# Optimization experiments

Hardware: AMD Instinct MI355X
Metric: run time of the kernel (lower is better)

## Reference

```python
import jax, jax.numpy as jnp
import numpy as np
from jax.scipy.special import logsumexp

D, V, B, N = 256, 10000, 16, 22
CF, CR, CA = 400, 120, 48   # num_func_cats, num_res_cats, num_arg_cats
NEG = -1e9


def setup_inputs() -> dict:
    key = jax.random.key(0)
    ks = jax.random.split(key, 12)
    s = 0.1
    return {
        "fake_emb": jnp.eye(CR, dtype=jnp.float32),  # nn.Parameter(torch.eye(num_res_cats))
        "nt_emb": jax.random.normal(ks[0], (CF, D), jnp.float32),
        "rule_W": jax.random.normal(ks[1], (2 * CA, CR), jnp.float32) * s,
        "rule_b": jnp.zeros((2 * CA,), jnp.float32),
        "root_w": jax.random.normal(ks[2], (CF,), jnp.float32) * s,  # root_mlp weight (input dim 1)
        "root_b": jnp.zeros((CF,), jnp.float32),
        "root_mask": jnp.zeros((CF,), jnp.float32),  # can_be_root mask (0 = allowed)
        "split_W1": jax.random.normal(ks[3], (D, D), jnp.float32) * s,
        "split_b1": jnp.zeros((D,), jnp.float32),
        "res_W": jax.random.normal(ks[4], (2, 2, D, D), jnp.float32) * s,  # 2 ResidualLayers x 2 Linears
        "res_b": jnp.zeros((2, 2, D), jnp.float32),
        "split_Wo": jax.random.normal(ks[5], (D, 2), jnp.float32) * s,
        "split_bo": jnp.zeros((2,), jnp.float32),
        "emit_W": jax.random.normal(ks[6], (D, V), jnp.float32) * s,  # word emission head
        "emit_b": jnp.zeros((V,), jnp.float32),
        "words": jax.random.randint(ks[7], (B, N), 0, V),
        "lfunc_ixs": jax.random.randint(ks[8], (CR, CA), 0, CF),
        "rfunc_ixs": jax.random.randint(ks[9], (CR, CA), 0, CF),
    }


def reference(fake_emb, nt_emb, rule_W, rule_b, root_w, root_b, root_mask,
              split_W1, split_b1, res_W, res_b, split_Wo, split_bo,
              emit_W, emit_b, words, lfunc_ixs, rfunc_ixs):
    # ---- grammar scores (set_grammar branch) ----
    # root_mlp(eye(1)).squeeze() == root_w + root_b
    root_scores = jax.nn.log_softmax(root_mask + root_w + root_b)          # [CF]
    rule_scores = jax.nn.log_softmax(fake_emb @ rule_W.T + rule_b, axis=1)  # [CR, 2*CA]

    # split_mlp: Linear -> ResidualLayer x2 -> Linear(D,2)
    h = nt_emb @ split_W1 + split_b1
    for i in range(2):  # fixed small layer loop
        t = jax.nn.relu(h @ res_W[i, 0] + res_b[i, 0])
        h = jax.nn.relu(t @ res_W[i, 1] + res_b[i, 1]) + h
    split_scores = jax.nn.log_softmax(h @ split_Wo + split_bo, axis=1)      # [CF, 2]

    gL = rule_scores[:, :CA] + split_scores[:CR, 0:1]  # full_G_larg [CR, CA]
    gR = rule_scores[:, CA:] + split_scores[:CR, 0:1]  # full_G_rarg [CR, CA]

    # ---- emission model: log p(word | category) gathered per token ----
    word_lp = jax.nn.log_softmax(nt_emb @ emit_W + emit_b, axis=-1)  # [CF, V]
    emit = word_lp[:, words]                                         # [CF, B, N]
    term = (split_scores[:, 1][:, None, None] + emit).transpose(2, 1, 0)  # [N, B, CF]

    # ---- CKY inside pass: beta[i, j, b, cat] over spans ----
    beta = jnp.full((N, N, B, CF), NEG, jnp.float32)
    d = jnp.arange(N)
    beta = beta.at[d, d].set(term)

    for w in range(2, N + 1):  # recurrence over span widths (static)
        S = N - w + 1
        st = np.arange(S)[:, None]          # span starts [S,1]
        kk = np.arange(1, w)[None, :]       # split points [1,w-1]
        left = beta[st, st + kk - 1]                                   # [S,w-1,B,CF]
        right = beta[st + kk, np.broadcast_to(st + w - 1, (S, w - 1))]  # [S,w-1,B,CF]
        # res -> arg(left) + rfunc(right)
        sL = gL + left[..., :CA][..., None, :] + right[..., rfunc_ixs]  # [S,w-1,B,CR,CA]
        # res -> lfunc(left) + arg(right)
        sR = gR + left[..., lfunc_ixs] + right[..., :CA][..., None, :]
        new = jnp.logaddexp(logsumexp(sL, axis=(1, 4)),
                            logsumexp(sR, axis=(1, 4)))                 # [S,B,CR]
        full = jnp.full((S, B, CF), NEG, jnp.float32).at[..., :CR].set(new)
        beta = beta.at[st[:, 0], st[:, 0] + w - 1].set(full)

    ll = logsumexp(root_scores + beta[0, N - 1], axis=-1)  # [B]
    return -ll  # logprob_list * -1
```

## Files before the change

kernel.cpp:

```cpp
#include <hip/hip_runtime.h>
#include <math.h>

#define D 256
#define V 10000
#define BB 16
#define NN 22
#define CF 400
#define CR 120
#define CA 48
#define CRP 121
#define PADF 20

#define RT 8
#define MLPB 200
__global__ __launch_bounds__(512) void k_mlp_emit(const float* __restrict__ nt_emb,
                      const float* __restrict__ W1, const float* __restrict__ b1,
                      const float* __restrict__ resW, const float* __restrict__ resb,
                      const float* __restrict__ Wo, const float* __restrict__ bo,
                      const float* __restrict__ emit_W, const float* __restrict__ emit_b,
                      float* __restrict__ split_scores, float* __restrict__ partial) {
  int bid = blockIdx.x;
  int t = threadIdx.x;
  if (bid < MLPB) {
    __shared__ float xs[2][D], hs[2][D], ts[2][D], prt[2][2][D];
    __shared__ float redg[2][4][2];
    int c = t & 255; int h = t >> 8;
    int f0 = bid * 2;
    xs[h][c] = nt_emb[(size_t)(f0 + h) * D + c];
    __syncthreads();
    int d0 = h * 128;
    float a0 = 0.f, a1 = 0.f;
#pragma unroll 8
    for (int dd = 0; dd < 128; dd++) {
      float wv = W1[(size_t)(d0 + dd) * D + c];
      a0 += xs[0][d0 + dd] * wv; a1 += xs[1][d0 + dd] * wv;
    }
    prt[0][h][c] = a0; prt[1][h][c] = a1;
    __syncthreads();
    if (h == 0) {
      float bv = b1[c];
      hs[0][c] = prt[0][0][c] + prt[0][1][c] + bv;
      hs[1][c] = prt[1][0][c] + prt[1][1][c] + bv;
    }
    __syncthreads();
    for (int il = 0; il < 2; il++) {
      const float* W = resW + (size_t)(il * 2) * D * D;
      a0 = 0.f; a1 = 0.f;
#pragma unroll 8
      for (int dd = 0; dd < 128; dd++) {
        float wv = W[(size_t)(d0 + dd) * D + c];
        a0 += hs[0][d0 + dd] * wv; a1 += hs[1][d0 + dd] * wv;
      }
      prt[0][h][c] = a0; prt[1][h][c] = a1;
      __syncthreads();
      if (h == 0) {
        float bv = resb[(il * 2) * D + c];
        ts[0][c] = fmaxf(prt[0][0][c] + prt[0][1][c] + bv, 0.f);
        ts[1][c] = fmaxf(prt[1][0][c] + prt[1][1][c] + bv, 0.f);
      }
      __syncthreads();
      const float* W2 = resW + (size_t)(il * 2 + 1) * D * D;
      a0 = 0.f; a1 = 0.f;
#pragma unroll 8
      for (int dd = 0; dd < 128; dd++) {
        float wv = W2[(size_t)(d0 + dd) * D + c];
        a0 += ts[0][d0 + dd] * wv; a1 += ts[1][d0 + dd] * wv;
      }
      prt[0][h][c] = a0; prt[1][h][c] = a1;
      __syncthreads();
      if (h == 0) {
        float bv = resb[(il * 2 + 1) * D + c];
        hs[0][c] = fmaxf(prt[0][0][c] + prt[0][1][c] + bv, 0.f) + hs[0][c];
        hs[1][c] = fmaxf(prt[1][0][c] + prt[1][1][c] + bv, 0.f) + hs[1][c];
      }
      __syncthreads();
    }
    float y0 = hs[h][c] * Wo[c * 2 + 0], y1 = hs[h][c] * Wo[c * 2 + 1];
    for (int off = 32; off; off >>= 1) { y0 += __shfl_down(y0, off, 64); y1 += __shfl_down(y1, off, 64); }
    int wq = (t >> 6) & 3;
    if ((t & 63) == 0) { redg[h][wq][0] = y0; redg[h][wq][1] = y1; }
    __syncthreads();
    if (c == 0) {
      float s0 = redg[h][0][0] + redg[h][1][0] + redg[h][2][0] + redg[h][3][0] + bo[0];
      float s1 = redg[h][0][1] + redg[h][1][1] + redg[h][2][1] + redg[h][3][1] + bo[1];
      float m = fmaxf(s0, s1);
      float z = m + __logf(__expf(s0 - m) + __expf(s1 - m));
      split_scores[(f0 + h) * 2 + 0] = s0 - z;
      split_scores[(f0 + h) * 2 + 1] = s1 - z;
    }
  } else {
    __shared__ float exs[RT][D];
    __shared__ float ldsw[RT][8];
    int e = bid - MLPB;
    int y = e / 50;
    int xt = e % 50;
    int f0 = xt * RT;
    int v0 = y * 2048 + t * 4;
    for (int idx = t; idx < RT * D; idx += 512) {
      int ri = idx >> 8, d = idx & 255;
      exs[ri][d] = nt_emb[(size_t)(f0 + ri) * D + d];
    }
    __syncthreads();
    float psum[RT];
    for (int ri = 0; ri < RT; ri++) psum[ri] = 0.f;
    if (v0 < V) {
      float acc[RT][4];
#pragma unroll
      for (int ri = 0; ri < RT; ri++)
        for (int j = 0; j < 4; j++) acc[ri][j] = 0.f;
      for (int d4 = 0; d4 < D / 4; d4++) {
        float4 w0 = *(const float4*)(emit_W + (size_t)(4 * d4 + 0) * V + v0);
        float4 w1 = *(const float4*)(emit_W + (size_t)(4 * d4 + 1) * V + v0);
        float4 w2 = *(const float4*)(emit_W + (size_t)(4 * d4 + 2) * V + v0);
        float4 w3 = *(const float4*)(emit_W + (size_t)(4 * d4 + 3) * V + v0);
#pragma unroll
        for (int ri = 0; ri < RT; ri++) {
          float4 xv = *(const float4*)(&exs[ri][4 * d4]);
          acc[ri][0] += xv.x * w0.x + xv.y * w1.x + xv.z * w2.x + xv.w * w3.x;
          acc[ri][1] += xv.x * w0.y + xv.y * w1.y + xv.z * w2.y + xv.w * w3.y;
          acc[ri][2] += xv.x * w0.z + xv.y * w1.z + xv.z * w2.z + xv.w * w3.z;
          acc[ri][3] += xv.x * w0.w + xv.y * w1.w + xv.z * w2.w + xv.w * w3.w;
        }
      }
      float4 eb = *(const float4*)(emit_b + v0);
#pragma unroll
      for (int ri = 0; ri < RT; ri++)
        psum[ri] = __expf(acc[ri][0] + eb.x) + __expf(acc[ri][1] + eb.y) +
                   __expf(acc[ri][2] + eb.z) + __expf(acc[ri][3] + eb.w);
    }
    int lane = t & 63, wid = t >> 6;
    for (int ri = 0; ri < RT; ri++) {
      float v = psum[ri];
      for (int off = 32; off; off >>= 1) v += __shfl_down(v, off, 64);
      if (lane == 0) ldsw[ri][wid] = v;
    }
    __syncthreads();
    if (t < RT) {
      float s = 0.f;
      for (int wv = 0; wv < 8; wv++) s += ldsw[t][wv];
      partial[(f0 + t) * 8 + y] = s;
    }
  }
}

__global__ void k_glgr(const float* __restrict__ rule_W, const float* __restrict__ rule_b,
                       const float* __restrict__ split_scores,
                       const int* __restrict__ lf, const int* __restrict__ rf,
                       const float* __restrict__ partialE, float* __restrict__ logZ,
                       float4* __restrict__ rules) {
  __shared__ float red[128];
  __shared__ float shv[96];
  int r = blockIdx.x;
  int t = threadIdx.x;
  if (r == CR) {
    for (int f = t; f < CF; f += 128) {
      float s = 0.f;
      for (int ct = 0; ct < 5; ct++) s += partialE[f * 8 + ct];
      logZ[f] = __logf(s);
    }
    return;
  }
  float x = (t < 96) ? (rule_W[t * CR + r] + rule_b[t]) : -INFINITY;
  red[t] = x; __syncthreads();
  for (int off = 64; off; off >>= 1) { if (t < off) red[t] = fmaxf(red[t], red[t + off]); __syncthreads(); }
  float m = red[0]; __syncthreads();
  red[t] = (t < 96) ? __expf(x - m) : 0.f; __syncthreads();
  for (int off = 64; off; off >>= 1) { if (t < off) red[t] += red[t + off]; __syncthreads(); }
  float z = m + __logf(red[0]);
  float s0 = split_scores[r * 2 + 0];
  if (t < 96) shv[t] = __expf((x - z) + s0);
  __syncthreads();
  if (t < CA) {
    float4 pk;
    pk.x = shv[t];
    pk.y = shv[CA + t];
    pk.z = __int_as_float(rf[r * CA + t]);
    pk.w = __int_as_float(lf[r * CA + t]);
    rules[r * CA + t] = pk;
  }
}

__global__ __launch_bounds__(512) void k_term(const float* __restrict__ nt_emb,
                       const float* __restrict__ emit_W,
                       const float* __restrict__ emit_b, const int* __restrict__ words,
                       const float* __restrict__ split_scores, const float* __restrict__ logZ,
                       float* __restrict__ ET, float* __restrict__ bmax) {
  __shared__ float vals[CF];
  __shared__ float redw[8];
  __shared__ float mfin;
  int blk = blockIdx.x;
  int b = blk / NN, n = blk % NN;
  int t = threadIdx.x;
  int lane = t & 63, wid = t >> 6;
  int wd = words[b * NN + n];
  float wc0 = emit_W[(size_t)(4 * lane + 0) * V + wd];
  float wc1 = emit_W[(size_t)(4 * lane + 1) * V + wd];
  float wc2 = emit_W[(size_t)(4 * lane + 2) * V + wd];
  float wc3 = emit_W[(size_t)(4 * lane + 3) * V + wd];
  float eb = emit_b[wd];
  float vmax = -INFINITY;
  int fbase = wid * 50;
  for (int k = 0; k < 50; k += 2) {
    int f0 = fbase + k, f1 = f0 + 1;
    float4 xa = *(const float4*)(nt_emb + (size_t)f0 * D + 4 * lane);
    float4 xb = *(const float4*)(nt_emb + (size_t)f1 * D + 4 * lane);
    float va = xa.x * wc0 + xa.y * wc1 + xa.z * wc2 + xa.w * wc3;
    float vb = xb.x * wc0 + xb.y * wc1 + xb.z * wc2 + xb.w * wc3;
    for (int off = 32; off; off >>= 1) {
      va += __shfl_down(va, off, 64);
      vb += __shfl_down(vb, off, 64);
    }
    if (lane == 0) {
      float fa = split_scores[f0 * 2 + 1] + (va + eb) - logZ[f0];
      float fb = split_scores[f1 * 2 + 1] + (vb + eb) - logZ[f1];
      vals[f0] = fa; vals[f1] = fb;
      vmax = fmaxf(vmax, fmaxf(fa, fb));
    }
  }
  if (lane == 0) redw[wid] = vmax;
  __syncthreads();
  if (t == 0) {
    float m = redw[0];
    for (int i2 = 1; i2 < 8; i2++) m = fmaxf(m, redw[i2]);
    mfin = m;
    bmax[(n * NN + n) * BB + b] = m;
  }
  __syncthreads();
  float m = mfin;
  for (int f = t; f < CF; f += 512) ET[((size_t)n * CF + f) * BB + b] = __expf(vals[f] - m);
}

__global__ __launch_bounds__(512) void k_cky_part(const float4* __restrict__ rules,
                      const float* __restrict__ ET, const float* __restrict__ EB,
                      const float* __restrict__ bmax, float* __restrict__ partial,
                      int w, int rsplit) {
  __shared__ float SL[CF * PADF];
  __shared__ float SR[CF * PADF];
  __shared__ float sMbuf[21 * BB];
  __shared__ float cks[BB];
  __shared__ float4 sred[512];
  int t = threadIdx.x;
  int blk = blockIdx.x;
  int rb = blk % rsplit; int rem = blk / rsplit;
  int wm1 = w - 1;
  int k = rem % wm1; int s = rem / wm1;
  int i = s, j = s + w - 1;
  bool ld = (k == 0), rd = (k == wm1 - 1);
  if (t < BB * wm1) {
    int k2 = t >> 4, b2 = t & 15;
    sMbuf[t] = bmax[(i * NN + (i + k2)) * BB + b2] + bmax[((i + k2 + 1) * NN + j) * BB + b2];
  }
  __syncthreads();
  if (t < BB) {
    float M = sMbuf[t];
    for (int k2 = 1; k2 < wm1; k2++) M = fmaxf(M, sMbuf[k2 * BB + t]);
    cks[t] = __expf(sMbuf[k * BB + t] - M);
  }
  const float* srcL = ld ? (ET + (size_t)i * CF * BB) : (EB + (size_t)(i * NN + (i + k)) * CRP * BB);
  const float* srcR = rd ? (ET + (size_t)j * CF * BB) : (EB + (size_t)((i + k + 1) * NN + j) * CRP * BB);
  int rowsL = ld ? CF : CRP, rowsR = rd ? CF : CRP;
  for (int idx = t; idx < rowsL * 4; idx += 512) {
    int f = idx >> 2, q = idx & 3;
    *(float4*)&SL[f * PADF + q * 4] = *(const float4*)&srcL[f * BB + q * 4];
  }
  for (int idx = t; idx < rowsR * 4; idx += 512) {
    int f = idx >> 2, q = idx & 3;
    *(float4*)&SR[f * PADF + q * 4] = *(const float4*)&srcR[f * BB + q * 4];
  }
  __syncthreads();
  int nr = CR / rsplit;
  int asplit = 128 / nr;
  int bq = t & 3, rr = t >> 2;
  float4 acc = {0.f, 0.f, 0.f, 0.f};
  bool act = (rr < nr * asplit);
  int rloc = rr % nr, asub = rr / nr;
  int r = rb * nr + rloc;
  if (act) {
    int na = CA / asplit;
    const float4* rp = rules + (size_t)r * CA + asub * na;
    int boff = bq * 4;
    int aB = asub * na;
#pragma unroll 4
    for (int a0 = 0; a0 < na; a0++) {
      float4 rule = rp[a0];
      int a = aB + a0;
      int fL = __float_as_int(rule.z);
      int fR = __float_as_int(rule.w);
      int fLc = rd ? fL : min(fL, 120);
      int fRc = ld ? fR : min(fR, 120);
      float4 La = *(const float4*)&SL[a * PADF + boff];
      float4 Ra = *(const float4*)&SR[a * PADF + boff];
      float4 Rg = *(const float4*)&SR[fLc * PADF + boff];
      float4 Lg = *(const float4*)&SL[fRc * PADF + boff];
      acc.x += rule.x * (La.x * Rg.x) + rule.y * (Lg.x * Ra.x);
      acc.y += rule.x * (La.y * Rg.y) + rule.y * (Lg.y * Ra.y);
      acc.z += rule.x * (La.z * Rg.z) + rule.y * (Lg.z * Ra.z);
      acc.w += rule.x * (La.w * Rg.w) + rule.y * (Lg.w * Ra.w);
    }
  }
  if (asplit > 1) {
    sred[t] = acc;
    __syncthreads();
    if (act && asub == 0) {
      for (int s2 = 1; s2 < asplit; s2++) {
        float4 o = sred[t + s2 * nr * 4];
        acc.x += o.x; acc.y += o.y; acc.z += o.z; acc.w += o.w;
      }
    }
  }
  if (act && asub == 0) {
    float4 c4 = *(const float4*)&cks[bq * 4];
    acc.x *= c4.x; acc.y *= c4.y; acc.z *= c4.z; acc.w *= c4.w;
    *(float4*)&partial[(((size_t)s * 21 + k) * CR + r) * BB + bq * 4] = acc;
  }
}

__global__ __launch_bounds__(512) void k_cky_comb(const float* __restrict__ partial,
                      float* __restrict__ EB, float* __restrict__ bmax, int w) {
  __shared__ float sums[CR * BB];
  __shared__ float sMbuf[21 * BB];
  __shared__ float msum[BB];
  __shared__ float Mb[BB];
  int t = threadIdx.x;
  int s = blockIdx.x;
  int i = s, j = s + w - 1;
  int wm1 = w - 1;
  if (t < BB * wm1) {
    int k2 = t >> 4, b2 = t & 15;
    sMbuf[t] = bmax[(i * NN + (i + k2)) * BB + b2] + bmax[((i + k2 + 1) * NN + j) * BB + b2];
  }
  __syncthreads();
  if (t < BB) {
    float M = sMbuf[t];
    for (int k2 = 1; k2 < wm1; k2++) M = fmaxf(M, sMbuf[k2 * BB + t]);
    Mb[t] = M;
  }
  int bq = t & 3, rr = t >> 2;
  float4 sum = {0.f, 0.f, 0.f, 0.f};
  if (rr < CR) {
    for (int k2 = 0; k2 < wm1; k2++) {
      float4 p = *(const float4*)&partial[(((size_t)s * 21 + k2) * CR + rr) * BB + bq * 4];
      sum.x += p.x; sum.y += p.y; sum.z += p.z; sum.w += p.w;
    }
    *(float4*)&sums[rr * BB + bq * 4] = sum;
  }
  __syncthreads();
  if (t < BB) {
    float m = 0.f;
    for (int r2 = 0; r2 < CR; r2++) m = fmaxf(m, sums[r2 * BB + t]);
    m = fmaxf(m, 1e-35f);
    msum[t] = m;
    bmax[(i * NN + j) * BB + t] = Mb[t] + __logf(m);
  }
  __syncthreads();
  if (rr < CR) {
    float4 m4 = *(const float4*)&msum[bq * 4];
    sum.x /= m4.x; sum.y /= m4.y; sum.z /= m4.z; sum.w /= m4.w;
    *(float4*)&EB[(((size_t)i * NN + j) * CRP + rr) * BB + bq * 4] = sum;
  }
  if (t < BB) EB[(((size_t)i * NN + j) * CRP + 120) * BB + t] = 0.f;
}

__global__ __launch_bounds__(128) void k_final(const float* __restrict__ root_w,
                        const float* __restrict__ root_b, const float* __restrict__ root_mask,
                        const float* __restrict__ EB, const float* __restrict__ bmax,
                        float* __restrict__ out) {
  __shared__ float red[128];
  int b = blockIdx.x;
  int t = threadIdx.x;
  float xv[4];
  float lm = -INFINITY;
  for (int kq = 0; kq < 4; kq++) {
    int f = t + kq * 128;
    xv[kq] = (f < CF) ? (root_mask[f] + root_w[f] + root_b[f]) : -INFINITY;
    lm = fmaxf(lm, xv[kq]);
  }
  red[t] = lm; __syncthreads();
  for (int off = 64; off; off >>= 1) { if (t < off) red[t] = fmaxf(red[t], red[t + off]); __syncthreads(); }
  float M = red[0]; __syncthreads();
  float le = 0.f;
  for (int kq = 0; kq < 4; kq++) le += (t + kq * 128 < CF) ? __expf(xv[kq] - M) : 0.f;
  red[t] = le; __syncthreads();
  for (int off = 64; off; off >>= 1) { if (t < off) red[t] += red[t + off]; __syncthreads(); }
  float z = M + __logf(red[0]);
  __syncthreads();
  float x = (t < CR) ? __expf(xv[0] - z) * EB[(((size_t)0 * NN + (NN - 1)) * CRP + t) * BB + b] : 0.f;
  red[t] = x; __syncthreads();
  for (int off = 64; off; off >>= 1) { if (t < off) red[t] += red[t + off]; __syncthreads(); }
  if (t == 0) out[b] = -(bmax[(0 * NN + (NN - 1)) * BB + b] + __logf(red[0]));
}

extern "C" void kernel_launch(void* const* d_in, const int* in_sizes, int n_in,
                              void* d_out, int out_size, void* d_ws, size_t ws_size,
                              hipStream_t stream) {
  const float* nt_emb   = (const float*)d_in[1];
  const float* rule_W   = (const float*)d_in[2];
  const float* rule_b   = (const float*)d_in[3];
  const float* root_w   = (const float*)d_in[4];
  const float* root_b   = (const float*)d_in[5];
  const float* root_mask= (const float*)d_in[6];
  const float* split_W1 = (const float*)d_in[7];
  const float* split_b1 = (const float*)d_in[8];
  const float* res_W    = (const float*)d_in[9];
  const float* res_b    = (const float*)d_in[10];
  const float* split_Wo = (const float*)d_in[11];
  const float* split_bo = (const float*)d_in[12];
  const float* emit_W   = (const float*)d_in[13];
  const float* emit_b   = (const float*)d_in[14];
  const int*   words    = (const int*)d_in[15];
  const int*   lfunc    = (const int*)d_in[16];
  const int*   rfunc    = (const int*)d_in[17];

  float* ws = (float*)d_ws;
  float* ET           = ws;
  float* EB           = ET + NN * CF * BB;
  float* bmaxbuf      = EB + NN * NN * CRP * BB;
  float* partialK     = bmaxbuf + NN * NN * BB;
  float* rules        = partialK + 21 * 21 * CR * BB;
  float* split_scores = rules + CR * CA * 4;
  float* logZ         = split_scores + 2 * CF;
  float* partialE     = logZ + CF;

  hipLaunchKernelGGL(k_mlp_emit, dim3(MLPB + 250), dim3(512), 0, stream, nt_emb,
                     split_W1, split_b1, res_W, res_b, split_Wo, split_bo,
                     emit_W, emit_b, split_scores, partialE);
  hipLaunchKernelGGL(k_glgr, dim3(CR + 1), dim3(128), 0, stream, rule_W, rule_b, split_scores,
                     lfunc, rfunc, partialE, logZ, (float4*)rules);
  hipLaunchKernelGGL(k_term, dim3(BB * NN), dim3(512), 0, stream, nt_emb, emit_W, emit_b,
                     words, split_scores, logZ, ET, bmaxbuf);
  for (int w = 2; w <= NN; w++) {
    int S = NN - w + 1;
    int units = S * (w - 1);
    int rsplit = (units >= 224) ? 1 : ((units >= 112) ? 2 : ((units >= 56) ? 4 : 8));
    hipLaunchKernelGGL(k_cky_part, dim3(units * rsplit), dim3(512), 0, stream,
                       (const float4*)rules, ET, EB, bmaxbuf, partialK, w, rsplit);
    hipLaunchKernelGGL(k_cky_comb, dim3(S), dim3(512), 0, stream, partialK, EB, bmaxbuf, w);
  }
  hipLaunchKernelGGL(k_final, dim3(BB), dim3(128), 0, stream, root_w, root_b, root_mask,
                     EB, bmaxbuf, (float*)d_out);
}
```

Before: 349.3 us.

## Fuse CKY part/combine into one step kernel that precomputes next width's middle splits

```diff
diff --git a/kernel.cpp b/kernel.cpp
--- a/kernel.cpp
+++ b/kernel.cpp
@@ -230,135 +230,198 @@
   for (int f = t; f < CF; f += 512) ET[((size_t)n * CF + f) * BB + b] = __expf(vals[f] - m);
 }
 
-__global__ __launch_bounds__(512) void k_cky_part(const float4* __restrict__ rules,
-                      const float* __restrict__ ET, const float* __restrict__ EB,
-                      const float* __restrict__ bmax, float* __restrict__ partial,
-                      int w, int rsplit) {
-  __shared__ float SL[CF * PADF];
-  __shared__ float SR[CF * PADF];
-  __shared__ float sMbuf[21 * BB];
-  __shared__ float cks[BB];
-  __shared__ float4 sred[512];
+__global__ __launch_bounds__(512) void k_cky_step(const float4* __restrict__ rules,
+                      const float* __restrict__ ET, float* __restrict__ EB,
+                      float* __restrict__ bmax, float* __restrict__ partA,
+                      float* __restrict__ partB, int w, int S, int rsplit) {
+  __shared__ float lds[21000];
+  __shared__ float sM[21 * BB];
+  __shared__ float Mb[BB];
+  __shared__ float msum[BB];
   int t = threadIdx.x;
-  int blk = blockIdx.x;
-  int rb = blk % rsplit; int rem = blk / rsplit;
-  int wm1 = w - 1;
-  int k = rem % wm1; int s = rem / wm1;
-  int i = s, j = s + w - 1;
-  bool ld = (k == 0), rd = (k == wm1 - 1);
-  if (t < BB * wm1) {
-    int k2 = t >> 4, b2 = t & 15;
-    sMbuf[t] = bmax[(i * NN + (i + k2)) * BB + b2] + bmax[((i + k2 + 1) * NN + j) * BB + b2];
-  }
-  __syncthreads();
-  if (t < BB) {
-    float M = sMbuf[t];
-    for (int k2 = 1; k2 < wm1; k2++) M = fmaxf(M, sMbuf[k2 * BB + t]);
-    cks[t] = __expf(sMbuf[k * BB + t] - M);
-  }
-  const float* srcL = ld ? (ET + (size_t)i * CF * BB) : (EB + (size_t)(i * NN + (i + k)) * CRP * BB);
-  const float* srcR = rd ? (ET + (size_t)j * CF * BB) : (EB + (size_t)((i + k + 1) * NN + j) * CRP * BB);
-  int rowsL = ld ? CF : CRP, rowsR = rd ? CF : CRP;
-  for (int idx = t; idx < rowsL * 4; idx += 512) {
-    int f = idx >> 2, q = idx & 3;
-    *(float4*)&SL[f * PADF + q * 4] = *(const float4*)&srcL[f * BB + q * 4];
-  }
-  for (int idx = t; idx < rowsR * 4; idx += 512) {
-    int f = idx >> 2, q = idx & 3;
-    *(float4*)&SR[f * PADF + q * 4] = *(const float4*)&srcR[f * BB + q * 4];
-  }
-  __syncthreads();
-  int nr = CR / rsplit;
-  int asplit = 128 / nr;
+  int bid = blockIdx.x;
   int bq = t & 3, rr = t >> 2;
-  float4 acc = {0.f, 0.f, 0.f, 0.f};
-  bool act = (rr < nr * asplit);
-  int rloc = rr % nr, asub = rr / nr;
-  int r = rb * nr + rloc;
-  if (act) {
-    int na = CA / asplit;
-    const float4* rp = rules + (size_t)r * CA + asub * na;
-    int boff = bq * 4;
-    int aB = asub * na;
+  if (bid < S) {
+    int s = bid, i = s, j = s + w - 1;
+    int wm1 = w - 1;
+    const float* partCur = (w & 1) ? partA : partB;
+    if (t < wm1 * BB) {
+      int k2 = t >> 4, b2 = t & 15;
+      sM[k2 * BB + b2] = bmax[((size_t)i * NN + (i + k2)) * BB + b2] +
+                         bmax[((size_t)(i + k2 + 1) * NN + j) * BB + b2];
+    }
+    __syncthreads();
+    if (t < BB) {
+      float M = sM[t];
+      for (int k2 = 1; k2 < wm1; k2++) M = fmaxf(M, sM[k2 * BB + t]);
+      Mb[t] = M;
+    }
+    float* SLe0 = lds;
+    float* SRe0 = lds + 8000;
+    float* SLe1 = lds + 10420;
+    float* SRe1 = lds + 12840;
+    for (int idx = t; idx < CF * 4; idx += 512) {
+      int f = idx >> 2, q = idx & 3;
+      *(float4*)&SLe0[f * PADF + q * 4] = *(const float4*)&ET[((size_t)i * CF + f) * BB + q * 4];
+    }
+    if (w == 2) {
+      for (int idx = t; idx < CF * 4; idx += 512) {
+        int f = idx >> 2, q = idx & 3;
+        *(float4*)&SRe0[f * PADF + q * 4] = *(const float4*)&ET[((size_t)j * CF + f) * BB + q * 4];
+      }
+    } else {
+      for (int idx = t; idx < CRP * 4; idx += 512) {
+        int f = idx >> 2, q = idx & 3;
+        *(float4*)&SRe0[f * PADF + q * 4] = *(const float4*)&EB[(((size_t)(i + 1) * NN + j) * CRP + f) * BB + q * 4];
+        *(float4*)&SLe1[f * PADF + q * 4] = *(const float4*)&EB[(((size_t)i * NN + (j - 1)) * CRP + f) * BB + q * 4];
+      }
+      for (int idx = t; idx < CF * 4; idx += 512) {
+        int f = idx >> 2, q = idx & 3;
+        *(float4*)&SRe1[f * PADF + q * 4] = *(const float4*)&ET[((size_t)j * CF + f) * BB + q * 4];
+      }
+    }
+    __syncthreads();
+    float4 acc = {0.f, 0.f, 0.f, 0.f};
+    if (rr < CR) {
+      const float4* rp = rules + (size_t)rr * CA;
+      int boff = bq * 4;
+      {
+        float4 e = {0.f, 0.f, 0.f, 0.f};
+        bool rd = (w == 2);
 #pragma unroll 4
-    for (int a0 = 0; a0 < na; a0++) {
-      float4 rule = rp[a0];
-      int a = aB + a0;
-      int fL = __float_as_int(rule.z);
-      int fR = __float_as_int(rule.w);
-      int fLc = rd ? fL : min(fL, 120);
-      int fRc = ld ? fR : min(fR, 120);
-      float4 La = *(const float4*)&SL[a * PADF + boff];
-      float4 Ra = *(const float4*)&SR[a * PADF + boff];
-      float4 Rg = *(const float4*)&SR[fLc * PADF + boff];
-      float4 Lg = *(const float4*)&SL[fRc * PADF + boff];
-      acc.x += rule.x * (La.x * Rg.x) + rule.y * (Lg.x * Ra.x);
-      acc.y += rule.x * (La.y * Rg.y) + rule.y * (Lg.y * Ra.y);
-      acc.z += rule.x * (La.z * Rg.z) + rule.y * (Lg.z * Ra.z);
-      acc.w += rule.x * (La.w * Rg.w) + rule.y * (Lg.w * Ra.w);
-    }
-  }
-  if (asplit > 1) {
-    sred[t] = acc;
-    __syncthreads();
+        for (int a = 0; a < CA; a++) {
+          float4 rule = rp[a];
+          int fL = __float_as_int(rule.z);
+          int fR = __float_as_int(rule.w);
+          int fLc = rd ? fL : min(fL, 120);
+          float4 La = *(const float4*)&SLe0[a * PADF + boff];
+          float4 Ra = *(const float4*)&SRe0[a * PADF + boff];
+          float4 Rg = *(const float4*)&SRe0[fLc * PADF + boff];
+          float4 Lg = *(const float4*)&SLe0[fR * PADF + boff];
+          e.x += rule.x * (La.x * Rg.x) + rule.y * (Lg.x * Ra.x);
+          e.y += rule.x * (La.y * Rg.y) + rule.y * (Lg.y * Ra.y);
+          e.z += rule.x * (La.z * Rg.z) + rule.y * (Lg.z * Ra.z);
+          e.w += rule.x * (La.w * Rg.w) + rule.y * (Lg.w * Ra.w);
+        }
+        acc.x = e.x * __expf(sM[boff + 0] - Mb[boff + 0]);
+        acc.y = e.y * __expf(sM[boff + 1] - Mb[boff + 1]);
+        acc.z = e.z * __expf(sM[boff + 2] - Mb[boff + 2]);
+        acc.w = e.w * __expf(sM[boff + 3] - Mb[boff + 3]);
+      }
+      for (int k = 1; k <= w - 3; k++) {
+        float4 p = *(const float4*)&partCur[(((size_t)s * 21 + k) * CR + rr) * BB + boff];
+        acc.x += p.x * __expf(sM[k * BB + boff + 0] - Mb[boff + 0]);
+        acc.y += p.y * __expf(sM[k * BB + boff + 1] - Mb[boff + 1]);
+        acc.z += p.z * __expf(sM[k * BB + boff + 2] - Mb[boff + 2]);
+        acc.w += p.w * __expf(sM[k * BB + boff + 3] - Mb[boff + 3]);
+      }
+      if (w > 2) {
+        float4 e = {0.f, 0.f, 0.f, 0.f};
+#pragma unroll 4
+        for (int a = 0; a < CA; a++) {
+          float4 rule = rp[a];
+          int fL = __float_as_int(rule.z);
+          int fR = __float_as_int(rule.w);
+          int fRc = min(fR, 120);
+          float4 La = *(const float4*)&SLe1[a * PADF + boff];
+          float4 Ra = *(const float4*)&SRe1[a * PADF + boff];
+          float4 Rg = *(const float4*)&SRe1[fL * PADF + boff];
+          float4 Lg = *(const float4*)&SLe1[fRc * PADF + boff];
+          e.x += rule.x * (La.x * Rg.x) + rule.y * (Lg.x * Ra.x);
+          e.y += rule.x * (La.y * Rg.y) + rule.y * (Lg.y * Ra.y);
+          e.z += rule.x * (La.z * Rg.z) + rule.y * (Lg.z * Ra.z);
+          e.w += rule.x * (La.w * Rg.w) + rule.y * (Lg.w * Ra.w);
+        }
+        int kb = (w - 2) * BB + boff;
+        acc.x += e.x * __expf(sM[kb + 0] - Mb[boff + 0]);
+        acc.y += e.y * __expf(sM[kb + 1] - Mb[boff + 1]);
+        acc.z += e.z * __expf(sM[kb + 2] - Mb[boff + 2]);
+        acc.w += e.w * __expf(sM[kb + 3] - Mb[boff + 3]);
+      }
+    }
+    __syncthreads();
+    float* sums = lds;
+    if (rr < CR) {
+      sums[rr * BB + bq * 4 + 0] = acc.x;
+      sums[rr * BB + bq * 4 + 1] = acc.y;
+      sums[rr * BB + bq * 4 + 2] = acc.z;
+      sums[rr * BB + bq * 4 + 3] = acc.w;
+    }
+    __syncthreads();
+    if (t < BB) {
+      float m = 0.f;
+      for (int r2 = 0; r2 < CR; r2++) m = fmaxf(m, sums[r2 * BB + t]);
+      m = fmaxf(m, 1e-35f);
+      msum[t] = m;
+      bmax[((size_t)i * NN + j) * BB + t] = Mb[t] + __logf(m);
+    }
+    __syncthreads();
+    if (rr < CR) {
+      float4 o;
+      o.x = acc.x / msum[bq * 4 + 0];
+      o.y = acc.y / msum[bq * 4 + 1];
+      o.z = acc.z / msum[bq * 4 + 2];
+      o.w = acc.w / msum[bq * 4 + 3];
+      *(float4*)&EB[(((size_t)i * NN + j) * CRP + rr) * BB + bq * 4] = o;
+    }
+    if (t < BB) EB[(((size_t)i * NN + j) * CRP + 120) * BB + t] = 0.f;
+  } else {
+    int W = w + 1;
+    int nmidk = W - 3;
+    int e = bid - S;
+    int rb = e % rsplit; int rem = e / rsplit;
+    int k = 1 + rem % nmidk; int s = rem / nmidk;
+    int i = s, j = s + W - 1;
+    float* partNext = (W & 1) ? partA : partB;
+    float* SL = lds;
+    float* SR = lds + 2420;
+    float4* sred = (float4*)(lds + 4840);
+    for (int idx = t; idx < CRP * 4; idx += 512) {
+      int f = idx >> 2, q = idx & 3;
+      *(float4*)&SL[f * PADF + q * 4] = *(const float4*)&EB[(((size_t)i * NN + (i + k)) * CRP + f) * BB + q * 4];
+      *(float4*)&SR[f * PADF + q * 4] = *(const float4*)&EB[(((size_t)(i + k + 1) * NN + j) * CRP + f) * BB + q * 4];
+    }
+    __syncthreads();
+    int nr = CR / rsplit;
+    int asplit = 128 / nr;
+    float4 acc = {0.f, 0.f, 0.f, 0.f};
+    bool act = (rr < nr * asplit);
+    int rloc = rr % nr, asub = rr / nr;
+    int r = rb * nr + rloc;
+    if (act) {
+      int na = CA / asplit;
+      const float4* rp = rules + (size_t)r * CA + asub * na;
+      int boff = bq * 4;
+#pragma unroll 4
+      for (int a0 = 0; a0 < na; a0++) {
+        float4 rule = rp[a0];
+        int fLc = min(__float_as_int(rule.z), 120);
+        int fRc = min(__float_as_int(rule.w), 120);
+        int a = asub * na + a0;
+        float4 La = *(const float4*)&SL[a * PADF + boff];
+        float4 Ra = *(const float4*)&SR[a * PADF + boff];
+        float4 Rg = *(const float4*)&SR[fLc * PADF + boff];
+        float4 Lg = *(const float4*)&SL[fRc * PADF + boff];
+        acc.x += rule.x * (La.x * Rg.x) + rule.y * (Lg.x * Ra.x);
+        acc.y += rule.x * (La.y * Rg.y) + rule.y * (Lg.y * Ra.y);
+        acc.z += rule.x * (La.z * Rg.z) + rule.y * (Lg.z * Ra.z);
+        acc.w += rule.x * (La.w * Rg.w) + rule.y * (Lg.w * Ra.w);
+      }
+    }
+    if (asplit > 1) {
+      sred[t] = acc;
+      __syncthreads();
+      if (act && asub == 0) {
+        for (int s2 = 1; s2 < asplit; s2++) {
+          float4 o = sred[t + s2 * nr * 4];
+          acc.x += o.x; acc.y += o.y; acc.z += o.z; acc.w += o.w;
+        }
+      }
+    }
     if (act && asub == 0) {
-      for (int s2 = 1; s2 < asplit; s2++) {
-        float4 o = sred[t + s2 * nr * 4];
-        acc.x += o.x; acc.y += o.y; acc.z += o.z; acc.w += o.w;
-      }
-    }
-  }
-  if (act && asub == 0) {
-    float4 c4 = *(const float4*)&cks[bq * 4];
-    acc.x *= c4.x; acc.y *= c4.y; acc.z *= c4.z; acc.w *= c4.w;
-    *(float4*)&partial[(((size_t)s * 21 + k) * CR + r) * BB + bq * 4] = acc;
-  }
-}
-
-__global__ __launch_bounds__(512) void k_cky_comb(const float* __restrict__ partial,
-                      float* __restrict__ EB, float* __restrict__ bmax, int w) {
-  __shared__ float sums[CR * BB];
-  __shared__ float sMbuf[21 * BB];
-  __shared__ float msum[BB];
-  __shared__ float Mb[BB];
-  int t = threadIdx.x;
-  int s = blockIdx.x;
-  int i = s, j = s + w - 1;
-  int wm1 = w - 1;
-  if (t < BB * wm1) {
-    int k2 = t >> 4, b2 = t & 15;
-    sMbuf[t] = bmax[(i * NN + (i + k2)) * BB + b2] + bmax[((i + k2 + 1) * NN + j) * BB + b2];
-  }
-  __syncthreads();
-  if (t < BB) {
-    float M = sMbuf[t];
-    for (int k2 = 1; k2 < wm1; k2++) M = fmaxf(M, sMbuf[k2 * BB + t]);
-    Mb[t] = M;
-  }
-  int bq = t & 3, rr = t >> 2;
-  float4 sum = {0.f, 0.f, 0.f, 0.f};
-  if (rr < CR) {
-    for (int k2 = 0; k2 < wm1; k2++) {
-      float4 p = *(const float4*)&partial[(((size_t)s * 21 + k2) * CR + rr) * BB + bq * 4];
-      sum.x += p.x; sum.y += p.y; sum.z += p.z; sum.w += p.w;
-    }
-    *(float4*)&sums[rr * BB + bq * 4] = sum;
-  }
-  __syncthreads();
-  if (t < BB) {
-    float m = 0.f;
-    for (int r2 = 0; r2 < CR; r2++) m = fmaxf(m, sums[r2 * BB + t]);
-    m = fmaxf(m, 1e-35f);
-    msum[t] = m;
-    bmax[(i * NN + j) * BB + t] = Mb[t] + __logf(m);
-  }
-  __syncthreads();
-  if (rr < CR) {
-    float4 m4 = *(const float4*)&msum[bq * 4];
-    sum.x /= m4.x; sum.y /= m4.y; sum.z /= m4.z; sum.w /= m4.w;
-    *(float4*)&EB[(((size_t)i * NN + j) * CRP + rr) * BB + bq * 4] = sum;
-  }
-  if (t < BB) EB[(((size_t)i * NN + j) * CRP + 120) * BB + t] = 0.f;
+      *(float4*)&partNext[(((size_t)s * 21 + k) * CR + r) * BB + bq * 4] = acc;
+    }
+  }
 }
 
 __global__ __launch_bounds__(128) void k_final(const float* __restrict__ root_w,
@@ -415,8 +478,9 @@
   float* ET           = ws;
   float* EB           = ET + NN * CF * BB;
   float* bmaxbuf      = EB + NN * NN * CRP * BB;
-  float* partialK     = bmaxbuf + NN * NN * BB;
-  float* rules        = partialK + 21 * 21 * CR * BB;
+  float* partA        = bmaxbuf + NN * NN * BB;
+  float* partB        = partA + 21 * 21 * CR * BB;
+  float* rules        = partB + 21 * 21 * CR * BB;
   float* split_scores = rules + CR * CA * 4;
   float* logZ         = split_scores + 2 * CF;
   float* partialE     = logZ + CF;
@@ -430,11 +494,13 @@
                      words, split_scores, logZ, ET, bmaxbuf);
   for (int w = 2; w <= NN; w++) {
     int S = NN - w + 1;
-    int units = S * (w - 1);
-    int rsplit = (units >= 224) ? 1 : ((units >= 112) ? 2 : ((units >= 56) ? 4 : 8));
-    hipLaunchKernelGGL(k_cky_part, dim3(units * rsplit), dim3(512), 0, stream,
-                       (const float4*)rules, ET, EB, bmaxbuf, partialK, w, rsplit);
-    hipLaunchKernelGGL(k_cky_comb, dim3(S), dim3(512), 0, stream, partialK, EB, bmaxbuf, w);
+    int midu = 0, rsplit = 1;
+    if (w + 1 <= NN && w - 2 >= 1) {
+      midu = (NN - w) * (w - 2);
+      rsplit = (midu >= 224) ? 1 : ((midu >= 112) ? 2 : ((midu >= 56) ? 4 : 8));
+    }
+    hipLaunchKernelGGL(k_cky_step, dim3(S + midu * rsplit), dim3(512), 0, stream,
+                       (const float4*)rules, ET, EB, bmaxbuf, partA, partB, w, S, rsplit);
   }
   hipLaunchKernelGGL(k_final, dim3(BB), dim3(128), 0, stream, root_w, root_b, root_mask,
                      EB, bmaxbuf, (float*)d_out);
```

New measurement: 455.8 us. +30.5%, slower.
